# Kernel optimization log

Measured on AMD Instinct MI355X. Metric: run time of the kernel, lower is better.

Reference implementation:

```python
import jax, jax.numpy as jnp
import numpy as np

N = 100000       # nodes
E = 1600000      # edges (avg degree 16)
IN, HID, OUT = 128, 128, 64


def setup_inputs() -> dict:
    key = jax.random.key(0)
    ks = jax.random.split(key, 8)
    x = jax.random.normal(ks[0], (N, IN), dtype=jnp.float32)
    edge_index = jax.random.randint(ks[1], (2, E), 0, N, dtype=jnp.int32)
    # Glorot-style init like PyG GCNConv
    def glorot(k, fan_in, fan_out):
        s = jnp.sqrt(6.0 / (fan_in + fan_out))
        return jax.random.uniform(k, (fan_in, fan_out), jnp.float32, -s, s)
    return {
        "x": x,
        "edge_index": edge_index,
        "W1": glorot(ks[2], IN, HID),  "b1": jnp.zeros((HID,), jnp.float32),
        "W2": glorot(ks[3], HID, HID), "b2": jnp.zeros((HID,), jnp.float32),
        "W3": glorot(ks[4], HID, OUT), "b3": jnp.zeros((OUT,), jnp.float32),
    }


def _gcn_norm(edge_index, n_nodes, dtype):
    # add self-loops, compute symmetric normalization D^-1/2 (A+I) D^-1/2
    loops = jnp.arange(n_nodes, dtype=edge_index.dtype)
    src = jnp.concatenate([edge_index[0], loops])
    dst = jnp.concatenate([edge_index[1], loops])
    deg = jax.ops.segment_sum(jnp.ones(src.shape[0], dtype), dst, num_segments=n_nodes)
    dinv = jnp.where(deg > 0, jax.lax.rsqrt(deg), 0.0)
    norm = dinv[src] * dinv[dst]  # [E+N]
    return src, dst, norm


def _gcn_conv(h, W, b, src, dst, norm, n_nodes):
    h = h @ W                                  # [N, out]
    msg = h[src] * norm[:, None]               # gather + scale per edge
    out = jax.ops.segment_sum(msg, dst, num_segments=n_nodes)  # scatter-add
    return out + b


def reference(x, edge_index, W1, b1, W2, b2, W3, b3):
    n_nodes = x.shape[0]
    src, dst, norm = _gcn_norm(edge_index, n_nodes, x.dtype)
    # layer 1 + 2: conv -> relu -> dropout(eval = identity)
    h = jax.nn.relu(_gcn_conv(x, W1, b1, src, dst, norm, n_nodes))
    h = jax.nn.relu(_gcn_conv(h, W2, b2, src, dst, norm, n_nodes))
    # final layer, no activation
    return _gcn_conv(h, W3, b3, src, dst, norm, n_nodes)
```

## Files before the change

kernel.cpp:

```cpp
#include <hip/hip_runtime.h>
#include <hip/hip_fp16.h>


typedef _Float16 half8 __attribute__((ext_vector_type(8)));
typedef float floatx4 __attribute__((ext_vector_type(4)));

struct h4 { __half2 a, b; };

constexpr int CH = 4096;

__global__ __launch_bounds__(256) void k_chist(const int* __restrict__ edst,
                                               int* __restrict__ histM, int E) {
    __shared__ int h[512];
    int tid = threadIdx.x;
    for (int i = tid; i < 512; i += 256) h[i] = 0;
    __syncthreads();
    int base = blockIdx.x * CH, end = min(E, base + CH);
    for (int e = base + tid; e < end; e += 256)
        atomicAdd(&h[edst[e] >> 8], 1);
    __syncthreads();
    int* row = histM + (size_t)blockIdx.x * 512;
    for (int i = tid; i < 512; i += 256) row[i] = h[i];
}

__global__ __launch_bounds__(512) void k_cscan(const int* __restrict__ histM,
                                               int* __restrict__ boff,
                                               int* __restrict__ gbase, int nblk) {
    __shared__ int sh[512];
    int t = threadIdx.x;
    int tot = 0;
    for (int b = 0; b < nblk; b++) tot += histM[(size_t)b * 512 + t];
    int val = tot;
    sh[t] = val;
    __syncthreads();
    for (int off = 1; off < 512; off <<= 1) {
        int o = (t >= off) ? sh[t - off] : 0;
        __syncthreads();
        val += o;
        sh[t] = val;
        __syncthreads();
    }
    int gb = val - tot;
    gbase[t] = gb;
    if (t == 511) gbase[512] = val;
    int run = gb;
    for (int b = 0; b < nblk; b++) {
        boff[(size_t)b * 512 + t] = run;
        run += histM[(size_t)b * 512 + t];
    }
}

__global__ __launch_bounds__(256) void k_cscatter(const int* __restrict__ esrc,
                                                  const int* __restrict__ edst,
                                                  const int* __restrict__ boff,
                                                  unsigned* __restrict__ stage, int E) {
    __shared__ int cur[512];
    int tid = threadIdx.x;
    const int* row = boff + (size_t)blockIdx.x * 512;
    for (int i = tid; i < 512; i += 256) cur[i] = row[i];
    __syncthreads();
    int base = blockIdx.x * CH, end = min(E, base + CH);
    for (int e = base + tid; e < end; e += 256) {
        int s = esrc[e], d = edst[e];
        int pos = atomicAdd(&cur[d >> 8], 1);
        stage[pos] = ((unsigned)(d & 255) << 24) | (unsigned)s;
    }
}

__global__ __launch_bounds__(256) void k_ffine(const unsigned* __restrict__ stage,
                                               const int* __restrict__ gbase,
                                               unsigned* __restrict__ epk,
                                               int* __restrict__ offs,
                                               float* __restrict__ dinv,
                                               int n, int Etot) {
    int b = blockIdx.x, tid = threadIdx.x;
    int seg0 = gbase[b];
    int cnt = gbase[b + 1] - seg0;
    int node0 = b << 8, nn = min(256, n - node0);
    __shared__ int hist[256], sh[256], cur[256];
    hist[tid] = 0;
    __syncthreads();
    for (int i = tid; i < cnt; i += 256)
        atomicAdd(&hist[stage[seg0 + i] >> 24], 1);
    __syncthreads();
    int v = hist[tid];
    int val = v;
    sh[tid] = val;
    __syncthreads();
    for (int off = 1; off < 256; off <<= 1) {
        int o = (tid >= off) ? sh[tid - off] : 0;
        __syncthreads();
        val += o;
        sh[tid] = val;
        __syncthreads();
    }
    int excl = val - v;
    if (tid < nn) {
        offs[node0 + tid] = seg0 + excl;
        dinv[node0 + tid] = rsqrtf((float)(v + 1));
    }
    cur[tid] = seg0 + excl;
    __syncthreads();
    for (int i = tid; i < cnt; i += 256) {
        unsigned r = stage[seg0 + i];
        int pos = atomicAdd(&cur[r >> 24], 1);
        epk[pos] = r & 0x00FFFFFFu;
    }
    if (b == 0 && tid == 0) offs[n] = Etot;
}

__global__ void k_wfrag3(const float* __restrict__ W1, _Float16* __restrict__ Wf1,
                         const float* __restrict__ W2, _Float16* __restrict__ Wf2,
                         const float* __restrict__ W3, _Float16* __restrict__ Wf3) {
    int blk = blockIdx.x;
    const float* W;
    _Float16* Wf;
    int F;
    if (blk < 8)      { W = W1; Wf = Wf1; F = 128; blk -= 0; }
    else if (blk < 16){ W = W2; Wf = Wf2; F = 128; blk -= 8; }
    else              { W = W3; Wf = Wf3; F = 64;  blk -= 16; }
    int NT = F / 16;
    int tid = blk * 256 + threadIdx.x;
    if (tid >= 4 * NT * 64) return;
    int lane = tid & 63;
    int ct = (tid >> 6) % NT;
    int ks = tid / (64 * NT);
    int k0 = ks * 32 + (lane >> 4) * 8;
    int c  = ct * 16 + (lane & 15);
#pragma unroll
    for (int j = 0; j < 8; j++)
        Wf[(size_t)tid * 8 + j] = (_Float16)W[(k0 + j) * F + c];
}

template <int F, bool IN32>
__global__ __launch_bounds__(512) void k_gemm_mfma(const void* __restrict__ Hv,
                                                   const _Float16* __restrict__ Wf,
                                                   const float* __restrict__ dinv,
                                                   _Float16* __restrict__ T, int n) {
    constexpr int NT = F / 16;
    int wave = threadIdx.x >> 6, lane = threadIdx.x & 63;
    int row0 = blockIdx.x * 128 + wave * 16;
    int arow = min(row0 + (lane & 15), n - 1);
    int k0 = (lane >> 4) * 8;
    const _Float16* Hh = (const _Float16*)Hv;
    const float*    Hf = (const float*)Hv;
    floatx4 acc[NT];
#pragma unroll
    for (int t = 0; t < NT; t++) acc[t] = floatx4{0.f, 0.f, 0.f, 0.f};
#pragma unroll
    for (int ks = 0; ks < 4; ks++) {
        half8 a;
        if constexpr (IN32) {
            const float* p = Hf + (size_t)arow * 128 + ks * 32 + k0;
            float4 f0 = *(const float4*)p;
            float4 f1 = *(const float4*)(p + 4);
            a[0] = (_Float16)f0.x; a[1] = (_Float16)f0.y;
            a[2] = (_Float16)f0.z; a[3] = (_Float16)f0.w;
            a[4] = (_Float16)f1.x; a[5] = (_Float16)f1.y;
            a[6] = (_Float16)f1.z; a[7] = (_Float16)f1.w;
        } else {
            a = *(const half8*)(Hh + (size_t)arow * 128 + ks * 32 + k0);
        }
#pragma unroll
        for (int t = 0; t < NT; t++) {
            half8 b = *(const half8*)(Wf + ((size_t)(ks * NT + t) * 64 + lane) * 8);
            acc[t] = __builtin_amdgcn_mfma_f32_16x16x32_f16(a, b, acc[t], 0, 0, 0);
        }
    }
    int rbase = row0 + (lane >> 4) * 4;
    int cl = lane & 15;
#pragma unroll
    for (int r = 0; r < 4; r++) {
        int rr = rbase + r;
        if (rr < n) {
            float sc = dinv[rr];
#pragma unroll
            for (int t = 0; t < NT; t++)
                T[(size_t)rr * F + t * 16 + cl] = (_Float16)(acc[t][r] * sc);
        }
    }
}

template <int F, bool RELU, typename OT>
__global__ __launch_bounds__(256) void k_prop(const __half* __restrict__ T,
                                              const int* __restrict__ offs,
                                              const unsigned* __restrict__ epk,
                                              const float* __restrict__ dinv,
                                              const float* __restrict__ bias,
                                              OT* __restrict__ Out, int n) {
    constexpr int GRP = F / 4;
    int g  = (int)((blockIdx.x * blockDim.x + threadIdx.x) / GRP);
    int fl = threadIdx.x % GRP;
    if (g >= n) return;
    int j = offs[g], end = offs[g + 1];
    float a0 = 0.f, a1 = 0.f, a2 = 0.f, a3 = 0.f;
    for (; j + 4 <= end; j += 4) {
        unsigned s0 = epk[j + 0], s1 = epk[j + 1];
        unsigned s2 = epk[j + 2], s3 = epk[j + 3];
        h4 v0 = *(const h4*)&T[(size_t)s0 * F + fl * 4];
        h4 v1 = *(const h4*)&T[(size_t)s1 * F + fl * 4];
        h4 v2 = *(const h4*)&T[(size_t)s2 * F + fl * 4];
        h4 v3 = *(const h4*)&T[(size_t)s3 * F + fl * 4];
        float2 f0a = __half22float2(v0.a), f0b = __half22float2(v0.b);
        float2 f1a = __half22float2(v1.a), f1b = __half22float2(v1.b);
        float2 f2a = __half22float2(v2.a), f2b = __half22float2(v2.b);
        float2 f3a = __half22float2(v3.a), f3b = __half22float2(v3.b);
        a0 += f0a.x + f1a.x + f2a.x + f3a.x;
        a1 += f0a.y + f1a.y + f2a.y + f3a.y;
        a2 += f0b.x + f1b.x + f2b.x + f3b.x;
        a3 += f0b.y + f1b.y + f2b.y + f3b.y;
    }
    for (; j < end; j++) {
        unsigned s = epk[j];
        h4 v = *(const h4*)&T[(size_t)s * F + fl * 4];
        float2 fa = __half22float2(v.a), fb = __half22float2(v.b);
        a0 += fa.x;
        a1 += fa.y;
        a2 += fb.x;
        a3 += fb.y;
    }
    h4 vs = *(const h4*)&T[(size_t)g * F + fl * 4];
    float2 sa = __half22float2(vs.a), sb = __half22float2(vs.b);
    a0 += sa.x; a1 += sa.y;
    a2 += sb.x; a3 += sb.y;
    float dv = dinv[g];
    float4 b = *(const float4*)&bias[fl * 4];
    float r0 = a0 * dv + b.x;
    float r1 = a1 * dv + b.y;
    float r2 = a2 * dv + b.z;
    float r3 = a3 * dv + b.w;
    if (RELU) {
        r0 = fmaxf(r0, 0.f); r1 = fmaxf(r1, 0.f);
        r2 = fmaxf(r2, 0.f); r3 = fmaxf(r3, 0.f);
    }
    if constexpr (sizeof(OT) == 2) {
        h4 pk;
        pk.a = __floats2half2_rn(r0, r1);
        pk.b = __floats2half2_rn(r2, r3);
        *(h4*)&Out[(size_t)g * F + fl * 4] = pk;
    } else {
        *(float4*)&Out[(size_t)g * F + fl * 4] = float4{r0, r1, r2, r3};
    }
}

extern "C" void kernel_launch(void* const* d_in, const int* in_sizes, int n_in,
                              void* d_out, int out_size, void* d_ws, size_t ws_size,
                              hipStream_t stream) {
    const float* x  = (const float*)d_in[0];
    const int*   ei = (const int*)d_in[1];
    const float* W1 = (const float*)d_in[2];
    const float* b1 = (const float*)d_in[3];
    const float* W2 = (const float*)d_in[4];
    const float* b2 = (const float*)d_in[5];
    const float* W3 = (const float*)d_in[6];
    const float* b3 = (const float*)d_in[7];
    float* out = (float*)d_out;

    const int HID = in_sizes[3];
    const int IN  = in_sizes[2] / HID;
    const int N   = in_sizes[0] / IN;
    const int E   = in_sizes[1] / 2;
    const int NBC  = (N + 255) >> 8;
    const int NBLK = (E + CH - 1) / CH;

    const int* esrc = ei;
    const int* edst = ei + E;

    char* p = (char*)d_ws;
    auto alloc = [&](size_t bytes) {
        void* r = (void*)p;
        p += (bytes + 255) & ~(size_t)255;
        return r;
    };
    float*    dinv  = (float*)alloc((size_t)N * 4);
    int*      offs  = (int*)alloc((size_t)(N + 1) * 4);
    int*      histM = (int*)alloc((size_t)NBLK * 512 * 4);
    int*      boff  = (int*)alloc((size_t)NBLK * 512 * 4);
    int*      gbase = (int*)alloc((size_t)513 * 4);
    unsigned* stage = (unsigned*)alloc((size_t)E * 4);
    unsigned* epk   = (unsigned*)alloc((size_t)E * 4);
    _Float16* t0    = (_Float16*)alloc((size_t)N * 128 * 2);
    _Float16* h0    = (_Float16*)alloc((size_t)N * 128 * 2);
    _Float16* wf1   = (_Float16*)alloc((size_t)128 * 128 * 2);
    _Float16* wf2   = (_Float16*)alloc((size_t)128 * 128 * 2);
    _Float16* wf3   = (_Float16*)alloc((size_t)128 * 64 * 2);
    (void)ws_size; (void)n_in; (void)out_size;

    const int B = 256;
    k_chist<<<NBLK, B, 0, stream>>>(edst, histM, E);
    k_cscan<<<1, 512, 0, stream>>>(histM, boff, gbase, NBLK);
    k_cscatter<<<NBLK, B, 0, stream>>>(esrc, edst, boff, stage, E);
    k_ffine<<<NBC, B, 0, stream>>>(stage, gbase, epk, offs, dinv, N, E);
    k_wfrag3<<<20, B, 0, stream>>>(W1, wf1, W2, wf2, W3, wf3);

    const int gb    = (N + 127) / 128;
    const int pb128 = (int)(((size_t)N * 32 + B - 1) / B);
    const int pb64  = (int)(((size_t)N * 16 + B - 1) / B);
    k_gemm_mfma<128, true><<<gb, 512, 0, stream>>>(x, wf1, dinv, t0, N);
    k_prop<128, true, __half><<<pb128, B, 0, stream>>>((const __half*)t0, offs, epk, dinv, b1, (__half*)h0, N);
    k_gemm_mfma<128, false><<<gb, 512, 0, stream>>>(h0, wf2, dinv, t0, N);
    k_prop<128, true, __half><<<pb128, B, 0, stream>>>((const __half*)t0, offs, epk, dinv, b2, (__half*)h0, N);
    k_gemm_mfma<64, false><<<gb, 512, 0, stream>>>(h0, wf3, dinv, t0, N);
    k_prop<64, false, float><<<pb64, B, 0, stream>>>((const __half*)t0, offs, epk, dinv, b3, out, N);
}
```

Measured before the change: 444.8 us.

## Parallelize per-bucket block offset scan across 512 workgroups

Replaces the single-workgroup scan, which serially looped over all chunk histograms twice per bucket, with a two-level scan. One workgroup per bucket scans that bucket across chunks, a small kernel scans the bucket totals, and the scatter kernel adds the global base to the local offset. This removes a serial bottleneck on one CU at the cost of an extra launch. The new scan handles at most 512 chunks (2 per thread), which holds for E=1.6M with CH=4096 (391 chunks).

```diff
diff --git a/kernel.cpp b/kernel.cpp
--- a/kernel.cpp
+++ b/kernel.cpp
@@ -23,14 +23,38 @@
     for (int i = tid; i < 512; i += 256) row[i] = h[i];
 }
 
-__global__ __launch_bounds__(512) void k_cscan(const int* __restrict__ histM,
-                                               int* __restrict__ boff,
-                                               int* __restrict__ gbase, int nblk) {
+__global__ __launch_bounds__(256) void k_dscan(const int* __restrict__ histM,
+                                               int* __restrict__ boffL,
+                                               int* __restrict__ dtot, int nblk) {
+    int d = blockIdx.x;
+    int t = threadIdx.x;
+    __shared__ int sh[256];
+    int i0 = 2 * t, i1 = 2 * t + 1;
+    int v0 = (i0 < nblk) ? histM[(size_t)i0 * 512 + d] : 0;
+    int v1 = (i1 < nblk) ? histM[(size_t)i1 * 512 + d] : 0;
+    int tsum = v0 + v1;
+    int val = tsum;
+    sh[t] = val;
+    __syncthreads();
+    for (int off = 1; off < 256; off <<= 1) {
+        int o = (t >= off) ? sh[t - off] : 0;
+        __syncthreads();
+        val += o;
+        sh[t] = val;
+        __syncthreads();
+    }
+    int excl = val - tsum;
+    if (i0 < nblk) boffL[(size_t)i0 * 512 + d] = excl;
+    if (i1 < nblk) boffL[(size_t)i1 * 512 + d] = excl + v0;
+    if (t == 255) dtot[d] = val;
+}
+
+__global__ __launch_bounds__(512) void k_gscan(const int* __restrict__ dtot,
+                                               int* __restrict__ gbase) {
     __shared__ int sh[512];
     int t = threadIdx.x;
-    int tot = 0;
-    for (int b = 0; b < nblk; b++) tot += histM[(size_t)b * 512 + t];
-    int val = tot;
+    int v = dtot[t];
+    int val = v;
     sh[t] = val;
     __syncthreads();
     for (int off = 1; off < 512; off <<= 1) {
@@ -40,24 +64,19 @@
         sh[t] = val;
         __syncthreads();
     }
-    int gb = val - tot;
-    gbase[t] = gb;
+    gbase[t] = val - v;
     if (t == 511) gbase[512] = val;
-    int run = gb;
-    for (int b = 0; b < nblk; b++) {
-        boff[(size_t)b * 512 + t] = run;
-        run += histM[(size_t)b * 512 + t];
-    }
 }
 
 __global__ __launch_bounds__(256) void k_cscatter(const int* __restrict__ esrc,
                                                   const int* __restrict__ edst,
-                                                  const int* __restrict__ boff,
+                                                  const int* __restrict__ boffL,
+                                                  const int* __restrict__ gbase,
                                                   unsigned* __restrict__ stage, int E) {
     __shared__ int cur[512];
     int tid = threadIdx.x;
-    const int* row = boff + (size_t)blockIdx.x * 512;
-    for (int i = tid; i < 512; i += 256) cur[i] = row[i];
+    const int* row = boffL + (size_t)blockIdx.x * 512;
+    for (int i = tid; i < 512; i += 256) cur[i] = gbase[i] + row[i];
     __syncthreads();
     int base = blockIdx.x * CH, end = min(E, base + CH);
     for (int e = base + tid; e < end; e += 256) {
@@ -275,7 +294,8 @@
     float*    dinv  = (float*)alloc((size_t)N * 4);
     int*      offs  = (int*)alloc((size_t)(N + 1) * 4);
     int*      histM = (int*)alloc((size_t)NBLK * 512 * 4);
-    int*      boff  = (int*)alloc((size_t)NBLK * 512 * 4);
+    int*      boffL = (int*)alloc((size_t)NBLK * 512 * 4);
+    int*      dtot  = (int*)alloc((size_t)512 * 4);
     int*      gbase = (int*)alloc((size_t)513 * 4);
     unsigned* stage = (unsigned*)alloc((size_t)E * 4);
     unsigned* epk   = (unsigned*)alloc((size_t)E * 4);
@@ -288,8 +308,9 @@
 
     const int B = 256;
     k_chist<<<NBLK, B, 0, stream>>>(edst, histM, E);
-    k_cscan<<<1, 512, 0, stream>>>(histM, boff, gbase, NBLK);
-    k_cscatter<<<NBLK, B, 0, stream>>>(esrc, edst, boff, stage, E);
+    k_dscan<<<512, B, 0, stream>>>(histM, boffL, dtot, NBLK);
+    k_gscan<<<1, 512, 0, stream>>>(dtot, gbase);
+    k_cscatter<<<NBLK, B, 0, stream>>>(esrc, edst, boffL, gbase, stage, E);
     k_ffine<<<NBC, B, 0, stream>>>(stage, gbase, epk, offs, dinv, N, E);
     k_wfrag3<<<20, B, 0, stream>>>(W1, wf1, W2, wf2, W3, wf3);
 
```

Result: faster. 361.1 us (-18.8%).
